# Performance work log

Hardware: AMD Instinct MI355X
Metric: run time of the kernel (lower is better)

The kernel has to match this reference:

```python
import jax, jax.numpy as jnp
import numpy as np

B, C_IMG, H, W = 16, 512, 32, 32
C_AUD, K_LEN, N_HEADS = 512, 256, 8
HEAD_DIM = C_AUD // N_HEADS
EPS = 1e-5


def setup_inputs() -> dict:
    key = jax.random.key(0)
    ks = jax.random.split(key, 12)
    s_img = 1.0 / np.sqrt(C_IMG)
    s_aud = 1.0 / np.sqrt(C_AUD)
    return {
        "img_feat": jax.random.normal(ks[0], (B, C_IMG, H, W), jnp.float32),
        "audio_feat": jax.random.normal(ks[1], (B, K_LEN, C_AUD), jnp.float32),
        "Wq": jax.random.uniform(ks[2], (C_IMG, C_AUD), jnp.float32, -s_img, s_img),
        "bq": jnp.zeros((C_AUD,), jnp.float32),
        "Wk": jax.random.uniform(ks[3], (C_AUD, C_AUD), jnp.float32, -s_aud, s_aud),
        "bk": jnp.zeros((C_AUD,), jnp.float32),
        "Wv": jax.random.uniform(ks[4], (C_AUD, C_AUD), jnp.float32, -s_aud, s_aud),
        "bv": jnp.zeros((C_AUD,), jnp.float32),
        "Wo": jax.random.uniform(ks[5], (C_AUD, C_IMG), jnp.float32, -s_aud, s_aud),
        "bo": jnp.zeros((C_IMG,), jnp.float32),
        "gamma": jnp.ones((C_IMG,), jnp.float32),
        "beta": jnp.zeros((C_IMG,), jnp.float32),
    }


def reference(img_feat, audio_feat, Wq, bq, Wk, bk, Wv, bv, Wo, bo, gamma, beta):
    b, c, h, w = img_feat.shape
    # b c h w -> b (h w) c
    img_seq = img_feat.reshape(b, c, h * w).transpose(0, 2, 1)
    q = img_seq @ Wq + bq                      # [b, q, C_AUD]
    k = audio_feat @ Wk + bk                   # [b, k, C_AUD]
    v = audio_feat @ Wv + bv
    # split heads: b s (h d) -> b h s d
    def split(x):
        bs, s, _ = x.shape
        return x.reshape(bs, s, N_HEADS, HEAD_DIM).transpose(0, 2, 1, 3)
    qh, kh, vh = split(q), split(k), split(v)
    scale = HEAD_DIM ** -0.5
    scores = jnp.einsum('bhqd,bhkd->bhqk', qh, kh) * scale
    weights = jax.nn.softmax(scores, axis=-1)
    attn = jnp.einsum('bhqk,bhkd->bhqd', weights, vh)
    attn = attn.transpose(0, 2, 1, 3).reshape(b, h * w, C_AUD)
    proj = attn @ Wo + bo                      # [b, q, C_IMG]
    y = img_seq + proj
    mu = jnp.mean(y, axis=-1, keepdims=True)
    var = jnp.mean((y - mu) ** 2, axis=-1, keepdims=True)
    y = (y - mu) * jax.lax.rsqrt(var + EPS) * gamma + beta
    # b (h w) c -> b c h w
    return y.transpose(0, 2, 1).reshape(b, c, h, w)
```

## Files before the change

kernel.cpp:

```cpp
#include <hip/hip_runtime.h>
#include <cstddef>

#define B_SZ 16
#define HW 1024
#define CCH 512
#define K_LEN 256
#define N_HEADS 8
#define EPS 1e-5f

typedef __bf16 bf16;
typedef bf16 bf16x8 __attribute__((ext_vector_type(8)));
typedef bf16 bf16x4 __attribute__((ext_vector_type(4)));
typedef float f32x4 __attribute__((ext_vector_type(4)));

__device__ __forceinline__ void gl_lds16(const bf16* g, bf16* l) {
    __builtin_amdgcn_global_load_lds(
        (const __attribute__((address_space(1))) void*)g,
        (__attribute__((address_space(3))) void*)l, 16, 0, 0);
}

__global__ __launch_bounds__(256) void transpose_cast_img(
    const float* __restrict__ src, bf16* __restrict__ dst)
{
    const int b  = blockIdx.z;
    const int s0 = blockIdx.x * 64;
    const int c0 = blockIdx.y * 64;
    __shared__ bf16 T[64][72];
    const int tid = threadIdx.x;
    {
        const int r = tid >> 2, cs = (tid & 3) << 4;
        const float* sp = src + ((size_t)b * CCH + c0 + r) * HW + s0 + cs;
        #pragma unroll
        for (int i = 0; i < 4; ++i) {
            float4 f = *(const float4*)(sp + i * 4);
            T[r][cs + i*4 + 0] = (bf16)f.x;
            T[r][cs + i*4 + 1] = (bf16)f.y;
            T[r][cs + i*4 + 2] = (bf16)f.z;
            T[r][cs + i*4 + 3] = (bf16)f.w;
        }
    }
    __syncthreads();
    {
        const int ss = tid >> 2, ks = (tid & 3) << 4;
        bf16x8 a, b8;
        #pragma unroll
        for (int j = 0; j < 8; ++j) { a[j] = T[ks + j][ss]; b8[j] = T[ks + 8 + j][ss]; }
        bf16* dp = dst + ((size_t)b * HW + s0 + ss) * CCH + c0 + ks;
        *(bf16x8*)dp = a;
        *(bf16x8*)(dp + 8) = b8;
    }
}

__global__ __launch_bounds__(256) void transpose_cast_w(
    const float* __restrict__ Wq, const float* __restrict__ Wk,
    const float* __restrict__ Wv, const float* __restrict__ Wo,
    bf16* __restrict__ dst)
{
    const int w = blockIdx.z;
    const float* src = (w == 0) ? Wq : (w == 1) ? Wk : (w == 2) ? Wv : Wo;
    const int n0 = blockIdx.x * 64;
    const int k0 = blockIdx.y * 64;
    __shared__ bf16 T[64][72];
    const int tid = threadIdx.x;
    {
        const int r = tid >> 2, cs = (tid & 3) << 4;
        const float* sp = src + (size_t)(k0 + r) * CCH + n0 + cs;
        #pragma unroll
        for (int i = 0; i < 4; ++i) {
            float4 f = *(const float4*)(sp + i * 4);
            T[r][cs + i*4 + 0] = (bf16)f.x;
            T[r][cs + i*4 + 1] = (bf16)f.y;
            T[r][cs + i*4 + 2] = (bf16)f.z;
            T[r][cs + i*4 + 3] = (bf16)f.w;
        }
    }
    __syncthreads();
    {
        const int nn = tid >> 2, ks = (tid & 3) << 4;
        bf16x8 a, b8;
        #pragma unroll
        for (int j = 0; j < 8; ++j) { a[j] = T[ks + j][nn]; b8[j] = T[ks + 8 + j][nn]; }
        bf16* dp = dst + (size_t)w * CCH * CCH + (size_t)(n0 + nn) * CCH + k0 + ks;
        *(bf16x8*)dp = a;
        *(bf16x8*)(dp + 8) = b8;
    }
}

__global__ __launch_bounds__(256) void gemm_bf16_mfma(
    const bf16* __restrict__ A, const bf16* __restrict__ Bt,
    const float* __restrict__ bias, bf16* __restrict__ out)
{
    const int tid  = threadIdx.x;
    const int wave = tid >> 6, lane = tid & 63;
    const int m0 = blockIdx.x * 128;
    const int n0 = blockIdx.y * 128;
    const int l15 = lane & 15, quad = lane >> 4;
    const int wm = (wave >> 1) * 64, wn = (wave & 1) * 64;

    __shared__ bf16 As[128 * 32];
    __shared__ bf16 Bs[128 * 32];

    const int r16 = lane >> 2;
    const int ks  = (lane & 3) * 8;

    f32x4 acc[4][4];
    #pragma unroll
    for (int i = 0; i < 4; ++i)
        #pragma unroll
        for (int j = 0; j < 4; ++j)
            acc[i][j] = (f32x4){0.f, 0.f, 0.f, 0.f};

    for (int k0 = 0; k0 < 512; k0 += 32) {
        #pragma unroll
        for (int i = 0; i < 2; ++i) {
            const int c = wave * 2 + i;
            gl_lds16(A  + (size_t)(m0 + c * 16 + r16) * 512 + k0 + ks, &As[c * 512]);
            gl_lds16(Bt + (size_t)(n0 + c * 16 + r16) * 512 + k0 + ks, &Bs[c * 512]);
        }
        __syncthreads();
        bf16x8 af[4], bfr[4];
        #pragma unroll
        for (int i = 0; i < 4; ++i)
            af[i] = *(const bf16x8*)&As[(wm + i * 16 + l15) * 32 + quad * 8];
        #pragma unroll
        for (int j = 0; j < 4; ++j)
            bfr[j] = *(const bf16x8*)&Bs[(wn + j * 16 + l15) * 32 + quad * 8];
        #pragma unroll
        for (int i = 0; i < 4; ++i)
            #pragma unroll
            for (int j = 0; j < 4; ++j)
                acc[i][j] = __builtin_amdgcn_mfma_f32_16x16x32_bf16(bfr[j], af[i], acc[i][j], 0, 0, 0);
        __syncthreads();
    }

    #pragma unroll
    for (int j = 0; j < 4; ++j) {
        const int gn = n0 + wn + j * 16 + quad * 4;
        const f32x4 bv4 = *(const f32x4*)(bias + gn);
        #pragma unroll
        for (int i = 0; i < 4; ++i) {
            const int gm = m0 + wm + i * 16 + l15;
            bf16x4 ov;
            #pragma unroll
            for (int r = 0; r < 4; ++r) ov[r] = (bf16)(acc[i][j][r] + bv4[r]);
            *(bf16x4*)(out + (size_t)gm * 512 + gn) = ov;
        }
    }
}

__global__ __launch_bounds__(256) void gemm_kv_mfma(
    const float* __restrict__ audio,
    const bf16* __restrict__ Bt,
    const float* __restrict__ bk, const float* __restrict__ bv,
    bf16* __restrict__ khout, bf16* __restrict__ vtout)
{
    const int tid  = threadIdx.x;
    const int wave = tid >> 6, lane = tid & 63;
    const int m0 = blockIdx.x * 128;
    const int n0 = blockIdx.y * 128;
    const int l15 = lane & 15, quad = lane >> 4;
    const int wm = (wave >> 1) * 64, wn = (wave & 1) * 64;

    __shared__ bf16 As[128 * 32];
    __shared__ bf16 Bs[128 * 32];

    const int r16 = lane >> 2;
    const int ks  = (lane & 3) * 8;

    f32x4 acc[4][4];
    #pragma unroll
    for (int i = 0; i < 4; ++i)
        #pragma unroll
        for (int j = 0; j < 4; ++j)
            acc[i][j] = (f32x4){0.f, 0.f, 0.f, 0.f};

    for (int k0 = 0; k0 < 512; k0 += 32) {
        #pragma unroll
        for (int i = 0; i < 2; ++i) {
            const int c = wave * 2 + i;
            gl_lds16(Bt + (size_t)(n0 + c * 16 + r16) * 512 + k0 + ks, &Bs[c * 512]);
        }
        #pragma unroll
        for (int i = 0; i < 2; ++i) {
            const int u = tid + (i << 8);
            const int r = u >> 2, seg = (u & 3) << 3;
            const float* ap = audio + (size_t)(m0 + r) * 512 + k0 + seg;
            f32x4 a0 = *(const f32x4*)ap;
            f32x4 a1 = *(const f32x4*)(ap + 4);
            bf16x8 o;
            #pragma unroll
            for (int q = 0; q < 4; ++q) { o[q] = (bf16)a0[q]; o[q + 4] = (bf16)a1[q]; }
            *(bf16x8*)&As[r * 32 + seg] = o;
        }
        __syncthreads();
        bf16x8 af[4], bfr[4];
        #pragma unroll
        for (int i = 0; i < 4; ++i)
            af[i] = *(const bf16x8*)&As[(wm + i * 16 + l15) * 32 + quad * 8];
        #pragma unroll
        for (int j = 0; j < 4; ++j)
            bfr[j] = *(const bf16x8*)&Bs[(wn + j * 16 + l15) * 32 + quad * 8];
        #pragma unroll
        for (int i = 0; i < 4; ++i)
            #pragma unroll
            for (int j = 0; j < 4; ++j)
                acc[i][j] = __builtin_amdgcn_mfma_f32_16x16x32_bf16(af[i], bfr[j], acc[i][j], 0, 0, 0);
        __syncthreads();
    }

    #pragma unroll
    for (int j = 0; j < 4; ++j) {
        const int gn = n0 + wn + j * 16 + l15;
        if (gn < 512) {
            const int h = gn >> 6, d = gn & 63;
            const float bias = bk[gn];
            #pragma unroll
            for (int i = 0; i < 4; ++i) {
                const int gm = m0 + wm + i * 16 + quad * 4;
                const int b = gm >> 8, key = gm & 255;
                bf16* base = khout + ((((size_t)b * N_HEADS + h) * K_LEN) + key) * 64 + d;
                #pragma unroll
                for (int r = 0; r < 4; ++r)
                    base[(size_t)r * 64] = (bf16)(acc[i][j][r] + bias);
            }
        } else {
            const int ch = gn - 512;
            const int h = ch >> 6, d = ch & 63;
            const float bias = bv[ch];
            #pragma unroll
            for (int i = 0; i < 4; ++i) {
                const int gm = m0 + wm + i * 16 + quad * 4;
                const int b = gm >> 8, key = gm & 255;
                bf16x4 pk;
                #pragma unroll
                for (int r = 0; r < 4; ++r) pk[r] = (bf16)(acc[i][j][r] + bias);
                *(bf16x4*)(vtout + (((size_t)b * N_HEADS + h) * 64 + d) * K_LEN + key) = pk;
            }
        }
    }
}

__global__ __launch_bounds__(256) void attn_mfma(
    const bf16* __restrict__ q,
    const bf16* __restrict__ kh,
    const bf16* __restrict__ vt,
    bf16* __restrict__ o)
{
    const int bh = blockIdx.x;
    const int s0 = blockIdx.y * 64;
    const int tid = threadIdx.x;
    const int wave = tid >> 6, lane = tid & 63;
    const int l15 = lane & 15, quad = lane >> 4;
    const int b = bh >> 3, h = bh & 7;

    __shared__ bf16 KsPt[18432];
    __shared__ bf16 Vs[16896];

    const bf16* khb = kh + (size_t)bh * K_LEN * 64;
    const bf16* vtb = vt + (size_t)bh * 64 * K_LEN;

    #pragma unroll
    for (int i = 0; i < 8; ++i) {
        const int chunk = tid + (i << 8);
        const int key = chunk >> 3, dseg = (chunk & 7) << 3;
        *(bf16x8*)&KsPt[key * 72 + dseg] = *(const bf16x8*)(khb + key * 64 + dseg);
        const int d = chunk >> 5, kseg = (chunk & 31) << 3;
        *(bf16x8*)&Vs[d * 264 + kseg] = *(const bf16x8*)(vtb + d * 256 + kseg);
    }
    __syncthreads();

    const int qrow = s0 + wave * 16 + l15;
    const bf16* qp = q + ((size_t)(b * HW + qrow)) * 512 + h * 64 + quad * 8;
    const bf16x8 qf0 = *(const bf16x8*)qp;
    const bf16x8 qf1 = *(const bf16x8*)(qp + 32);

    f32x4 acc[16];
    #pragma unroll
    for (int m = 0; m < 16; ++m) acc[m] = (f32x4){0.f, 0.f, 0.f, 0.f};
    #pragma unroll
    for (int m = 0; m < 16; ++m) {
        const bf16x8 a0 = *(const bf16x8*)&KsPt[(m * 16 + l15) * 72 + quad * 8];
        const bf16x8 a1 = *(const bf16x8*)&KsPt[(m * 16 + l15) * 72 + 32 + quad * 8];
        acc[m] = __builtin_amdgcn_mfma_f32_16x16x32_bf16(a0, qf0, acc[m], 0, 0, 0);
        acc[m] = __builtin_amdgcn_mfma_f32_16x16x32_bf16(a1, qf1, acc[m], 0, 0, 0);
    }

    float mx = -1e30f;
    #pragma unroll
    for (int m = 0; m < 16; ++m)
        mx = fmaxf(mx, fmaxf(fmaxf(acc[m][0], acc[m][1]), fmaxf(acc[m][2], acc[m][3])));
    mx = fmaxf(mx, __shfl_xor(mx, 16, 64));
    mx = fmaxf(mx, __shfl_xor(mx, 32, 64));

    __syncthreads();

    bf16* PtW = &KsPt[wave * 4224];
    float l_sum = 0.f;
    #pragma unroll
    for (int m = 0; m < 16; ++m) {
        bf16x4 pk;
        #pragma unroll
        for (int r = 0; r < 4; ++r) {
            const float p = __expf((acc[m][r] - mx) * 0.125f);
            l_sum += p;
            pk[r] = (bf16)p;
        }
        *(bf16x4*)&PtW[l15 * 264 + m * 16 + quad * 4] = pk;
    }
    l_sum += __shfl_xor(l_sum, 16, 64);
    l_sum += __shfl_xor(l_sum, 32, 64);
    __syncthreads();

    f32x4 oacc[4];
    #pragma unroll
    for (int m = 0; m < 4; ++m) oacc[m] = (f32x4){0.f, 0.f, 0.f, 0.f};
    #pragma unroll
    for (int s = 0; s < 8; ++s) {
        const bf16x8 pb = *(const bf16x8*)&PtW[l15 * 264 + s * 32 + quad * 8];
        #pragma unroll
        for (int m = 0; m < 4; ++m) {
            const bf16x8 va = *(const bf16x8*)&Vs[(m * 16 + l15) * 264 + s * 32 + quad * 8];
            oacc[m] = __builtin_amdgcn_mfma_f32_16x16x32_bf16(va, pb, oacc[m], 0, 0, 0);
        }
    }

    const float inv = 1.0f / l_sum;
    bf16* op = o + ((size_t)(b * HW + qrow)) * 512 + h * 64 + quad * 4;
    #pragma unroll
    for (int m = 0; m < 4; ++m) {
        bf16x4 ov;
        #pragma unroll
        for (int r = 0; r < 4; ++r) ov[r] = (bf16)(oacc[m][r] * inv);
        *(bf16x4*)&op[m * 16] = ov;
    }
}

__global__ __launch_bounds__(256) void gemm_oln(
    const bf16* __restrict__ A,
    const bf16* __restrict__ Wt,
    const float* __restrict__ bo,
    const float* __restrict__ img,
    const float* __restrict__ gamma, const float* __restrict__ beta,
    float* __restrict__ out)
{
    const int tid  = threadIdx.x;
    const int wave = tid >> 6, lane = tid & 63;
    const int l15 = lane & 15, quad = lane >> 4;
    const int m0 = blockIdx.x * 32;
    const int b  = m0 >> 10, s0 = m0 & 1023;
    const int wn = wave * 128;

    __shared__ bf16 As[32 * 32];
    __shared__ bf16 Bs[512 * 32];
    __shared__ float redS[2][32][4];

    const int r16 = lane >> 2;
    const int ks  = (lane & 3) * 8;

    f32x4 acc[2][8];
    #pragma unroll
    for (int i = 0; i < 2; ++i)
        #pragma unroll
        for (int j = 0; j < 8; ++j)
            acc[i][j] = (f32x4){0.f, 0.f, 0.f, 0.f};

    for (int k0 = 0; k0 < 512; k0 += 32) {
        #pragma unroll
        for (int t = 0; t < 8; ++t) {
            const int cb = wave * 8 + t;
            gl_lds16(Wt + (size_t)(cb * 16 + r16) * 512 + k0 + ks, &Bs[cb * 512]);
        }
        if (wave < 2)
            gl_lds16(A + (size_t)(m0 + wave * 16 + r16) * 512 + k0 + ks, &As[wave * 512]);
        __syncthreads();
        bf16x8 af[2], bfr[8];
        #pragma unroll
        for (int i = 0; i < 2; ++i)
            af[i] = *(const bf16x8*)&As[(i * 16 + l15) * 32 + quad * 8];
        #pragma unroll
        for (int j = 0; j < 8; ++j)
            bfr[j] = *(const bf16x8*)&Bs[(wn + j * 16 + l15) * 32 + quad * 8];
        #pragma unroll
        for (int i = 0; i < 2; ++i)
            #pragma unroll
            for (int j = 0; j < 8; ++j)
                acc[i][j] = __builtin_amdgcn_mfma_f32_16x16x32_bf16(af[i], bfr[j], acc[i][j], 0, 0, 0);
        __syncthreads();
    }

    float rs_[2][4] = {}, rq_[2][4] = {};
    #pragma unroll
    for (int j = 0; j < 8; ++j) {
        const int c = wn + j * 16 + l15;
        const float bo_c = bo[c];
        #pragma unroll
        for (int i = 0; i < 2; ++i) {
            const int sb = s0 + i * 16 + quad * 4;
            const f32x4 res = *(const f32x4*)(img + ((size_t)b * CCH + c) * HW + sb);
            #pragma unroll
            for (int r = 0; r < 4; ++r) {
                const float y = acc[i][j][r] + bo_c + res[r];
                acc[i][j][r] = y;
                rs_[i][r] += y;
                rq_[i][r] += y * y;
            }
        }
    }
    #pragma unroll
    for (int i = 0; i < 2; ++i)
        #pragma unroll
        for (int r = 0; r < 4; ++r) {
            #pragma unroll
            for (int m = 1; m < 16; m <<= 1) {
                rs_[i][r] += __shfl_xor(rs_[i][r], m, 64);
                rq_[i][r] += __shfl_xor(rq_[i][r], m, 64);
            }
        }
    if (l15 == 0) {
        #pragma unroll
        for (int i = 0; i < 2; ++i)
            #pragma unroll
            for (int r = 0; r < 4; ++r) {
                redS[0][i * 16 + quad * 4 + r][wave] = rs_[i][r];
                redS[1][i * 16 + quad * 4 + r][wave] = rq_[i][r];
            }
    }
    __syncthreads();

    float mu[2][4], rstd[2][4];
    #pragma unroll
    for (int i = 0; i < 2; ++i)
        #pragma unroll
        for (int r = 0; r < 4; ++r) {
            const int s = i * 16 + quad * 4 + r;
            const float sm = redS[0][s][0] + redS[0][s][1] + redS[0][s][2] + redS[0][s][3];
            const float sq = redS[1][s][0] + redS[1][s][1] + redS[1][s][2] + redS[1][s][3];
            const float m_ = sm * (1.f / 512.f);
            mu[i][r] = m_;
            rstd[i][r] = rsqrtf(sq * (1.f / 512.f) - m_ * m_ + EPS);
        }

    #pragma unroll
    for (int j = 0; j < 8; ++j) {
        const int c = wn + j * 16 + l15;
        const float g_c = gamma[c];
        const float be_c = beta[c];
        #pragma unroll
        for (int i = 0; i < 2; ++i) {
            const int sb = s0 + i * 16 + quad * 4;
            f32x4 z;
            #pragma unroll
            for (int r = 0; r < 4; ++r)
                z[r] = (acc[i][j][r] - mu[i][r]) * rstd[i][r] * g_c + be_c;
            *(f32x4*)(out + ((size_t)b * CCH + c) * HW + sb) = z;
        }
    }
}

extern "C" void kernel_launch(void* const* d_in, const int* in_sizes, int n_in,
                              void* d_out, int out_size, void* d_ws, size_t ws_size,
                              hipStream_t stream) {
    const float* img   = (const float*)d_in[0];
    const float* audio = (const float*)d_in[1];
    const float* Wq    = (const float*)d_in[2];
    const float* bq    = (const float*)d_in[3];
    const float* Wk    = (const float*)d_in[4];
    const float* bk    = (const float*)d_in[5];
    const float* Wv    = (const float*)d_in[6];
    const float* bv    = (const float*)d_in[7];
    const float* Wo    = (const float*)d_in[8];
    const float* bo    = (const float*)d_in[9];
    const float* gamma = (const float*)d_in[10];
    const float* beta  = (const float*)d_in[11];

    bf16* wsb    = (bf16*)d_ws;
    bf16* img_bf = wsb;
    bf16* wT     = img_bf + 8388608;
    bf16* q_bf   = wT + 1048576;
    bf16* kh_bf  = q_bf + 8388608;
    bf16* vt_bf  = kh_bf + 2097152;
    bf16* a_bf   = vt_bf + 2097152;

    transpose_cast_img<<<dim3(16, 8, 16), 256, 0, stream>>>(img, img_bf);
    transpose_cast_w<<<dim3(8, 8, 4), 256, 0, stream>>>(Wq, Wk, Wv, Wo, wT);

    gemm_bf16_mfma<<<dim3(128, 4), 256, 0, stream>>>(img_bf, wT, bq, q_bf);
    gemm_kv_mfma<<<dim3(32, 8), 256, 0, stream>>>(audio, wT + 262144, bk, bv, kh_bf, vt_bf);
    attn_mfma<<<dim3(B_SZ * N_HEADS, HW / 64), 256, 0, stream>>>(q_bf, kh_bf, vt_bf, a_bf);
    gemm_oln<<<dim3(512), 256, 0, stream>>>(a_bf, wT + 3 * 262144, bo, img, gamma, beta, (float*)d_out);
}
```

Before: 204.2 us.

## Merge transpose and QKV launches, keep K in registers, read bf16 residual

Merges the two transpose-cast kernels into one launch and the Q and KV projection GEMMs into one launch, cutting the launch count from six to four. The attention kernel now holds K fragments in registers, stages P in shared memory per wave and loops over several query tiles per block, so each block loads K and V once for more queries. The output/LayerNorm kernel reads the residual from the bf16 transposed image instead of fp32 and uses a transposed MFMA layout, giving vector bias/gamma loads but scalar strided output stores. The bf16 residual reduces precision of the skip path.

```diff
diff --git a/kernel.cpp b/kernel.cpp
--- a/kernel.cpp
+++ b/kernel.cpp
@@ -19,90 +19,87 @@
         (__attribute__((address_space(3))) void*)l, 16, 0, 0);
 }
 
-__global__ __launch_bounds__(256) void transpose_cast_img(
-    const float* __restrict__ src, bf16* __restrict__ dst)
+__global__ __launch_bounds__(256) void tc_all(
+    const float* __restrict__ img,
+    const float* __restrict__ Wq, const float* __restrict__ Wk,
+    const float* __restrict__ Wv, const float* __restrict__ Wo,
+    bf16* __restrict__ img_bf, bf16* __restrict__ wT)
 {
-    const int b  = blockIdx.z;
-    const int s0 = blockIdx.x * 64;
-    const int c0 = blockIdx.y * 64;
     __shared__ bf16 T[64][72];
     const int tid = threadIdx.x;
-    {
-        const int r = tid >> 2, cs = (tid & 3) << 4;
-        const float* sp = src + ((size_t)b * CCH + c0 + r) * HW + s0 + cs;
-        #pragma unroll
-        for (int i = 0; i < 4; ++i) {
-            float4 f = *(const float4*)(sp + i * 4);
-            T[r][cs + i*4 + 0] = (bf16)f.x;
-            T[r][cs + i*4 + 1] = (bf16)f.y;
-            T[r][cs + i*4 + 2] = (bf16)f.z;
-            T[r][cs + i*4 + 3] = (bf16)f.w;
-        }
-    }
-    __syncthreads();
-    {
-        const int ss = tid >> 2, ks = (tid & 3) << 4;
-        bf16x8 a, b8;
-        #pragma unroll
-        for (int j = 0; j < 8; ++j) { a[j] = T[ks + j][ss]; b8[j] = T[ks + 8 + j][ss]; }
-        bf16* dp = dst + ((size_t)b * HW + s0 + ss) * CCH + c0 + ks;
-        *(bf16x8*)dp = a;
-        *(bf16x8*)(dp + 8) = b8;
-    }
-}
-
-__global__ __launch_bounds__(256) void transpose_cast_w(
-    const float* __restrict__ Wq, const float* __restrict__ Wk,
-    const float* __restrict__ Wv, const float* __restrict__ Wo,
-    bf16* __restrict__ dst)
+    const int z = blockIdx.z;
+    if (z < 16) {
+        const int b = z, s0 = blockIdx.x * 64, c0 = blockIdx.y * 64;
+        {
+            const int r = tid >> 2, cs = (tid & 3) << 4;
+            const float* sp = img + ((size_t)b * CCH + c0 + r) * HW + s0 + cs;
+            #pragma unroll
+            for (int i = 0; i < 4; ++i) {
+                float4 f = *(const float4*)(sp + i * 4);
+                T[r][cs + i*4 + 0] = (bf16)f.x;
+                T[r][cs + i*4 + 1] = (bf16)f.y;
+                T[r][cs + i*4 + 2] = (bf16)f.z;
+                T[r][cs + i*4 + 3] = (bf16)f.w;
+            }
+        }
+        __syncthreads();
+        {
+            const int ss = tid >> 2, ks = (tid & 3) << 4;
+            bf16x8 a, b8;
+            #pragma unroll
+            for (int j = 0; j < 8; ++j) { a[j] = T[ks + j][ss]; b8[j] = T[ks + 8 + j][ss]; }
+            bf16* dp = img_bf + ((size_t)b * HW + s0 + ss) * CCH + c0 + ks;
+            *(bf16x8*)dp = a;
+            *(bf16x8*)(dp + 8) = b8;
+        }
+    } else {
+        if (blockIdx.x >= 8) return;
+        const int w = z - 16;
+        const float* src = (w == 0) ? Wq : (w == 1) ? Wk : (w == 2) ? Wv : Wo;
+        const int n0 = blockIdx.x * 64, k0 = blockIdx.y * 64;
+        {
+            const int r = tid >> 2, cs = (tid & 3) << 4;
+            const float* sp = src + (size_t)(k0 + r) * CCH + n0 + cs;
+            #pragma unroll
+            for (int i = 0; i < 4; ++i) {
+                float4 f = *(const float4*)(sp + i * 4);
+                T[r][cs + i*4 + 0] = (bf16)f.x;
+                T[r][cs + i*4 + 1] = (bf16)f.y;
+                T[r][cs + i*4 + 2] = (bf16)f.z;
+                T[r][cs + i*4 + 3] = (bf16)f.w;
+            }
+        }
+        __syncthreads();
+        {
+            const int nn = tid >> 2, ks = (tid & 3) << 4;
+            bf16x8 a, b8;
+            #pragma unroll
+            for (int j = 0; j < 8; ++j) { a[j] = T[ks + j][nn]; b8[j] = T[ks + 8 + j][nn]; }
+            bf16* dp = wT + (size_t)w * CCH * CCH + (size_t)(n0 + nn) * CCH + k0 + ks;
+            *(bf16x8*)dp = a;
+            *(bf16x8*)(dp + 8) = b8;
+        }
+    }
+}
+
+__global__ __launch_bounds__(256) void gemm_qkv(
+    const bf16* __restrict__ img_bf, const float* __restrict__ audio,
+    const bf16* __restrict__ wT,
+    const float* __restrict__ bq, const float* __restrict__ bk,
+    const float* __restrict__ bv,
+    bf16* __restrict__ q_bf, bf16* __restrict__ khout, bf16* __restrict__ vtout)
 {
-    const int w = blockIdx.z;
-    const float* src = (w == 0) ? Wq : (w == 1) ? Wk : (w == 2) ? Wv : Wo;
-    const int n0 = blockIdx.x * 64;
-    const int k0 = blockIdx.y * 64;
-    __shared__ bf16 T[64][72];
+    const int bid = blockIdx.x;
     const int tid = threadIdx.x;
-    {
-        const int r = tid >> 2, cs = (tid & 3) << 4;
-        const float* sp = src + (size_t)(k0 + r) * CCH + n0 + cs;
-        #pragma unroll
-        for (int i = 0; i < 4; ++i) {
-            float4 f = *(const float4*)(sp + i * 4);
-            T[r][cs + i*4 + 0] = (bf16)f.x;
-            T[r][cs + i*4 + 1] = (bf16)f.y;
-            T[r][cs + i*4 + 2] = (bf16)f.z;
-            T[r][cs + i*4 + 3] = (bf16)f.w;
-        }
-    }
-    __syncthreads();
-    {
-        const int nn = tid >> 2, ks = (tid & 3) << 4;
-        bf16x8 a, b8;
-        #pragma unroll
-        for (int j = 0; j < 8; ++j) { a[j] = T[ks + j][nn]; b8[j] = T[ks + 8 + j][nn]; }
-        bf16* dp = dst + (size_t)w * CCH * CCH + (size_t)(n0 + nn) * CCH + k0 + ks;
-        *(bf16x8*)dp = a;
-        *(bf16x8*)(dp + 8) = b8;
-    }
-}
-
-__global__ __launch_bounds__(256) void gemm_bf16_mfma(
-    const bf16* __restrict__ A, const bf16* __restrict__ Bt,
-    const float* __restrict__ bias, bf16* __restrict__ out)
-{
-    const int tid  = threadIdx.x;
     const int wave = tid >> 6, lane = tid & 63;
-    const int m0 = blockIdx.x * 128;
-    const int n0 = blockIdx.y * 128;
     const int l15 = lane & 15, quad = lane >> 4;
     const int wm = (wave >> 1) * 64, wn = (wave & 1) * 64;
+    const int r16 = lane >> 2;
+    const int ks  = (lane & 3) * 8;
 
     __shared__ bf16 As[128 * 32];
     __shared__ bf16 Bs[128 * 32];
 
-    const int r16 = lane >> 2;
-    const int ks  = (lane & 3) * 8;
-
     f32x4 acc[4][4];
     #pragma unroll
     for (int i = 0; i < 4; ++i)
@@ -110,151 +107,128 @@
         for (int j = 0; j < 4; ++j)
             acc[i][j] = (f32x4){0.f, 0.f, 0.f, 0.f};
 
-    for (int k0 = 0; k0 < 512; k0 += 32) {
-        #pragma unroll
-        for (int i = 0; i < 2; ++i) {
-            const int c = wave * 2 + i;
-            gl_lds16(A  + (size_t)(m0 + c * 16 + r16) * 512 + k0 + ks, &As[c * 512]);
-            gl_lds16(Bt + (size_t)(n0 + c * 16 + r16) * 512 + k0 + ks, &Bs[c * 512]);
-        }
-        __syncthreads();
-        bf16x8 af[4], bfr[4];
-        #pragma unroll
-        for (int i = 0; i < 4; ++i)
-            af[i] = *(const bf16x8*)&As[(wm + i * 16 + l15) * 32 + quad * 8];
-        #pragma unroll
-        for (int j = 0; j < 4; ++j)
-            bfr[j] = *(const bf16x8*)&Bs[(wn + j * 16 + l15) * 32 + quad * 8];
-        #pragma unroll
-        for (int i = 0; i < 4; ++i)
+    if (bid < 512) {
+        const int m0 = (bid >> 2) * 128, n0 = (bid & 3) * 128;
+        for (int k0 = 0; k0 < 512; k0 += 32) {
+            #pragma unroll
+            for (int i = 0; i < 2; ++i) {
+                const int c = wave * 2 + i;
+                gl_lds16(img_bf + (size_t)(m0 + c * 16 + r16) * 512 + k0 + ks, &As[c * 512]);
+                gl_lds16(wT     + (size_t)(n0 + c * 16 + r16) * 512 + k0 + ks, &Bs[c * 512]);
+            }
+            __syncthreads();
+            bf16x8 af[4], bfr[4];
+            #pragma unroll
+            for (int i = 0; i < 4; ++i)
+                af[i] = *(const bf16x8*)&As[(wm + i * 16 + l15) * 32 + quad * 8];
             #pragma unroll
             for (int j = 0; j < 4; ++j)
-                acc[i][j] = __builtin_amdgcn_mfma_f32_16x16x32_bf16(bfr[j], af[i], acc[i][j], 0, 0, 0);
-        __syncthreads();
-    }
-
-    #pragma unroll
-    for (int j = 0; j < 4; ++j) {
-        const int gn = n0 + wn + j * 16 + quad * 4;
-        const f32x4 bv4 = *(const f32x4*)(bias + gn);
-        #pragma unroll
-        for (int i = 0; i < 4; ++i) {
-            const int gm = m0 + wm + i * 16 + l15;
-            bf16x4 ov;
-            #pragma unroll
-            for (int r = 0; r < 4; ++r) ov[r] = (bf16)(acc[i][j][r] + bv4[r]);
-            *(bf16x4*)(out + (size_t)gm * 512 + gn) = ov;
-        }
-    }
-}
-
-__global__ __launch_bounds__(256) void gemm_kv_mfma(
-    const float* __restrict__ audio,
-    const bf16* __restrict__ Bt,
-    const float* __restrict__ bk, const float* __restrict__ bv,
-    bf16* __restrict__ khout, bf16* __restrict__ vtout)
-{
-    const int tid  = threadIdx.x;
-    const int wave = tid >> 6, lane = tid & 63;
-    const int m0 = blockIdx.x * 128;
-    const int n0 = blockIdx.y * 128;
-    const int l15 = lane & 15, quad = lane >> 4;
-    const int wm = (wave >> 1) * 64, wn = (wave & 1) * 64;
-
-    __shared__ bf16 As[128 * 32];
-    __shared__ bf16 Bs[128 * 32];
-
-    const int r16 = lane >> 2;
-    const int ks  = (lane & 3) * 8;
-
-    f32x4 acc[4][4];
-    #pragma unroll
-    for (int i = 0; i < 4; ++i)
-        #pragma unroll
-        for (int j = 0; j < 4; ++j)
-            acc[i][j] = (f32x4){0.f, 0.f, 0.f, 0.f};
-
-    for (int k0 = 0; k0 < 512; k0 += 32) {
-        #pragma unroll
-        for (int i = 0; i < 2; ++i) {
-            const int c = wave * 2 + i;
-            gl_lds16(Bt + (size_t)(n0 + c * 16 + r16) * 512 + k0 + ks, &Bs[c * 512]);
-        }
-        #pragma unroll
-        for (int i = 0; i < 2; ++i) {
-            const int u = tid + (i << 8);
-            const int r = u >> 2, seg = (u & 3) << 3;
-            const float* ap = audio + (size_t)(m0 + r) * 512 + k0 + seg;
-            f32x4 a0 = *(const f32x4*)ap;
-            f32x4 a1 = *(const f32x4*)(ap + 4);
-            bf16x8 o;
-            #pragma unroll
-            for (int q = 0; q < 4; ++q) { o[q] = (bf16)a0[q]; o[q + 4] = (bf16)a1[q]; }
-            *(bf16x8*)&As[r * 32 + seg] = o;
-        }
-        __syncthreads();
-        bf16x8 af[4], bfr[4];
-        #pragma unroll
-        for (int i = 0; i < 4; ++i)
-            af[i] = *(const bf16x8*)&As[(wm + i * 16 + l15) * 32 + quad * 8];
-        #pragma unroll
-        for (int j = 0; j < 4; ++j)
-            bfr[j] = *(const bf16x8*)&Bs[(wn + j * 16 + l15) * 32 + quad * 8];
-        #pragma unroll
-        for (int i = 0; i < 4; ++i)
+                bfr[j] = *(const bf16x8*)&Bs[(wn + j * 16 + l15) * 32 + quad * 8];
+            #pragma unroll
+            for (int i = 0; i < 4; ++i)
+                #pragma unroll
+                for (int j = 0; j < 4; ++j)
+                    acc[i][j] = __builtin_amdgcn_mfma_f32_16x16x32_bf16(bfr[j], af[i], acc[i][j], 0, 0, 0);
+            __syncthreads();
+        }
+        #pragma unroll
+        for (int j = 0; j < 4; ++j) {
+            const int gn = n0 + wn + j * 16 + quad * 4;
+            const f32x4 bv4 = *(const f32x4*)(bq + gn);
+            #pragma unroll
+            for (int i = 0; i < 4; ++i) {
+                const int gm = m0 + wm + i * 16 + l15;
+                bf16x4 ov;
+                #pragma unroll
+                for (int r = 0; r < 4; ++r) ov[r] = (bf16)(acc[i][j][r] + bv4[r]);
+                *(bf16x4*)(q_bf + (size_t)gm * 512 + gn) = ov;
+            }
+        }
+    } else {
+        const int t = bid - 512;
+        const int m0 = (t >> 3) * 128, n0 = (t & 7) * 128;
+        const bf16* Bt = wT + 262144;
+        for (int k0 = 0; k0 < 512; k0 += 32) {
+            #pragma unroll
+            for (int i = 0; i < 2; ++i) {
+                const int c = wave * 2 + i;
+                gl_lds16(Bt + (size_t)(n0 + c * 16 + r16) * 512 + k0 + ks, &Bs[c * 512]);
+            }
+            #pragma unroll
+            for (int i = 0; i < 2; ++i) {
+                const int u = tid + (i << 8);
+                const int r = u >> 2, seg = (u & 3) << 3;
+                const float* ap = audio + (size_t)(m0 + r) * 512 + k0 + seg;
+                f32x4 a0 = *(const f32x4*)ap;
+                f32x4 a1 = *(const f32x4*)(ap + 4);
+                bf16x8 o;
+                #pragma unroll
+                for (int qq = 0; qq < 4; ++qq) { o[qq] = (bf16)a0[qq]; o[qq + 4] = (bf16)a1[qq]; }
+                *(bf16x8*)&As[r * 32 + seg] = o;
+            }
+            __syncthreads();
+            bf16x8 af[4], bfr[4];
+            #pragma unroll
+            for (int i = 0; i < 4; ++i)
+                af[i] = *(const bf16x8*)&As[(wm + i * 16 + l15) * 32 + quad * 8];
             #pragma unroll
             for (int j = 0; j < 4; ++j)
-                acc[i][j] = __builtin_amdgcn_mfma_f32_16x16x32_bf16(af[i], bfr[j], acc[i][j], 0, 0, 0);
-        __syncthreads();
-    }
-
-    #pragma unroll
-    for (int j = 0; j < 4; ++j) {
-        const int gn = n0 + wn + j * 16 + l15;
-        if (gn < 512) {
-            const int h = gn >> 6, d = gn & 63;
-            const float bias = bk[gn];
-            #pragma unroll
-            for (int i = 0; i < 4; ++i) {
-                const int gm = m0 + wm + i * 16 + quad * 4;
-                const int b = gm >> 8, key = gm & 255;
-                bf16* base = khout + ((((size_t)b * N_HEADS + h) * K_LEN) + key) * 64 + d;
-                #pragma unroll
-                for (int r = 0; r < 4; ++r)
-                    base[(size_t)r * 64] = (bf16)(acc[i][j][r] + bias);
-            }
-        } else {
-            const int ch = gn - 512;
-            const int h = ch >> 6, d = ch & 63;
-            const float bias = bv[ch];
-            #pragma unroll
-            for (int i = 0; i < 4; ++i) {
-                const int gm = m0 + wm + i * 16 + quad * 4;
-                const int b = gm >> 8, key = gm & 255;
-                bf16x4 pk;
-                #pragma unroll
-                for (int r = 0; r < 4; ++r) pk[r] = (bf16)(acc[i][j][r] + bias);
-                *(bf16x4*)(vtout + (((size_t)b * N_HEADS + h) * 64 + d) * K_LEN + key) = pk;
-            }
-        }
-    }
-}
-
-__global__ __launch_bounds__(256) void attn_mfma(
+                bfr[j] = *(const bf16x8*)&Bs[(wn + j * 16 + l15) * 32 + quad * 8];
+            #pragma unroll
+            for (int i = 0; i < 4; ++i)
+                #pragma unroll
+                for (int j = 0; j < 4; ++j)
+                    acc[i][j] = __builtin_amdgcn_mfma_f32_16x16x32_bf16(af[i], bfr[j], acc[i][j], 0, 0, 0);
+            __syncthreads();
+        }
+        #pragma unroll
+        for (int j = 0; j < 4; ++j) {
+            const int gn = n0 + wn + j * 16 + l15;
+            if (gn < 512) {
+                const int h = gn >> 6, d = gn & 63;
+                const float bias = bk[gn];
+                #pragma unroll
+                for (int i = 0; i < 4; ++i) {
+                    const int gm = m0 + wm + i * 16 + quad * 4;
+                    const int b = gm >> 8, key = gm & 255;
+                    bf16* base = khout + ((((size_t)b * N_HEADS + h) * K_LEN) + key) * 64 + d;
+                    #pragma unroll
+                    for (int r = 0; r < 4; ++r)
+                        base[(size_t)r * 64] = (bf16)(acc[i][j][r] + bias);
+                }
+            } else {
+                const int ch = gn - 512;
+                const int h = ch >> 6, d = ch & 63;
+                const float bias = bv[ch];
+                #pragma unroll
+                for (int i = 0; i < 4; ++i) {
+                    const int gm = m0 + wm + i * 16 + quad * 4;
+                    const int b = gm >> 8, key = gm & 255;
+                    bf16x4 pk;
+                    #pragma unroll
+                    for (int r = 0; r < 4; ++r) pk[r] = (bf16)(acc[i][j][r] + bias);
+                    *(bf16x4*)(vtout + (((size_t)b * N_HEADS + h) * 64 + d) * K_LEN + key) = pk;
+                }
+            }
+        }
+    }
+}
+
+__global__ __launch_bounds__(256, 2) void attn_mfma(
     const bf16* __restrict__ q,
     const bf16* __restrict__ kh,
     const bf16* __restrict__ vt,
     bf16* __restrict__ o)
 {
     const int bh = blockIdx.x;
-    const int s0 = blockIdx.y * 64;
+    const int sg = blockIdx.y;
     const int tid = threadIdx.x;
     const int wave = tid >> 6, lane = tid & 63;
     const int l15 = lane & 15, quad = lane >> 4;
     const int b = bh >> 3, h = bh & 7;
 
-    __shared__ bf16 KsPt[18432];
-    __shared__ bf16 Vs[16896];
+    __shared__ bf16 Vs[64 * 264];
+    __shared__ bf16 Pt[4 * 16 * 264];
 
     const bf16* khb = kh + (size_t)bh * K_LEN * 64;
     const bf16* vtb = vt + (size_t)bh * 64 * K_LEN;
@@ -262,76 +236,79 @@
     #pragma unroll
     for (int i = 0; i < 8; ++i) {
         const int chunk = tid + (i << 8);
-        const int key = chunk >> 3, dseg = (chunk & 7) << 3;
-        *(bf16x8*)&KsPt[key * 72 + dseg] = *(const bf16x8*)(khb + key * 64 + dseg);
         const int d = chunk >> 5, kseg = (chunk & 31) << 3;
         *(bf16x8*)&Vs[d * 264 + kseg] = *(const bf16x8*)(vtb + d * 256 + kseg);
     }
+    bf16x8 kf0[16], kf1[16];
+    #pragma unroll
+    for (int m = 0; m < 16; ++m) {
+        const bf16* kp = khb + (size_t)(m * 16 + l15) * 64 + quad * 8;
+        kf0[m] = *(const bf16x8*)kp;
+        kf1[m] = *(const bf16x8*)(kp + 32);
+    }
     __syncthreads();
 
-    const int qrow = s0 + wave * 16 + l15;
-    const bf16* qp = q + ((size_t)(b * HW + qrow)) * 512 + h * 64 + quad * 8;
-    const bf16x8 qf0 = *(const bf16x8*)qp;
-    const bf16x8 qf1 = *(const bf16x8*)(qp + 32);
-
-    f32x4 acc[16];
-    #pragma unroll
-    for (int m = 0; m < 16; ++m) acc[m] = (f32x4){0.f, 0.f, 0.f, 0.f};
-    #pragma unroll
-    for (int m = 0; m < 16; ++m) {
-        const bf16x8 a0 = *(const bf16x8*)&KsPt[(m * 16 + l15) * 72 + quad * 8];
-        const bf16x8 a1 = *(const bf16x8*)&KsPt[(m * 16 + l15) * 72 + 32 + quad * 8];
-        acc[m] = __builtin_amdgcn_mfma_f32_16x16x32_bf16(a0, qf0, acc[m], 0, 0, 0);
-        acc[m] = __builtin_amdgcn_mfma_f32_16x16x32_bf16(a1, qf1, acc[m], 0, 0, 0);
-    }
-
-    float mx = -1e30f;
-    #pragma unroll
-    for (int m = 0; m < 16; ++m)
-        mx = fmaxf(mx, fmaxf(fmaxf(acc[m][0], acc[m][1]), fmaxf(acc[m][2], acc[m][3])));
-    mx = fmaxf(mx, __shfl_xor(mx, 16, 64));
-    mx = fmaxf(mx, __shfl_xor(mx, 32, 64));
-
-    __syncthreads();
-
-    bf16* PtW = &KsPt[wave * 4224];
-    float l_sum = 0.f;
-    #pragma unroll
-    for (int m = 0; m < 16; ++m) {
-        bf16x4 pk;
-        #pragma unroll
-        for (int r = 0; r < 4; ++r) {
-            const float p = __expf((acc[m][r] - mx) * 0.125f);
-            l_sum += p;
-            pk[r] = (bf16)p;
-        }
-        *(bf16x4*)&PtW[l15 * 264 + m * 16 + quad * 4] = pk;
-    }
-    l_sum += __shfl_xor(l_sum, 16, 64);
-    l_sum += __shfl_xor(l_sum, 32, 64);
-    __syncthreads();
-
-    f32x4 oacc[4];
-    #pragma unroll
-    for (int m = 0; m < 4; ++m) oacc[m] = (f32x4){0.f, 0.f, 0.f, 0.f};
-    #pragma unroll
-    for (int s = 0; s < 8; ++s) {
-        const bf16x8 pb = *(const bf16x8*)&PtW[l15 * 264 + s * 32 + quad * 8];
+    bf16* PtW = &Pt[wave * 4224];
+
+    for (int it = 0; it < 4; ++it) {
+        const int qrow = sg * 256 + it * 64 + wave * 16 + l15;
+        const bf16* qp = q + ((size_t)(b * HW + qrow)) * 512 + h * 64 + quad * 8;
+        const bf16x8 qf0 = *(const bf16x8*)qp;
+        const bf16x8 qf1 = *(const bf16x8*)(qp + 32);
+
+        f32x4 acc[16];
+        #pragma unroll
+        for (int m = 0; m < 16; ++m) acc[m] = (f32x4){0.f, 0.f, 0.f, 0.f};
+        #pragma unroll
+        for (int m = 0; m < 16; ++m) {
+            acc[m] = __builtin_amdgcn_mfma_f32_16x16x32_bf16(kf0[m], qf0, acc[m], 0, 0, 0);
+            acc[m] = __builtin_amdgcn_mfma_f32_16x16x32_bf16(kf1[m], qf1, acc[m], 0, 0, 0);
+        }
+
+        float mx = -1e30f;
+        #pragma unroll
+        for (int m = 0; m < 16; ++m)
+            mx = fmaxf(mx, fmaxf(fmaxf(acc[m][0], acc[m][1]), fmaxf(acc[m][2], acc[m][3])));
+        mx = fmaxf(mx, __shfl_xor(mx, 16, 64));
+        mx = fmaxf(mx, __shfl_xor(mx, 32, 64));
+
+        float l_sum = 0.f;
+        #pragma unroll
+        for (int m = 0; m < 16; ++m) {
+            bf16x4 pk;
+            #pragma unroll
+            for (int r = 0; r < 4; ++r) {
+                const float p = __expf((acc[m][r] - mx) * 0.125f);
+                l_sum += p;
+                pk[r] = (bf16)p;
+            }
+            *(bf16x4*)&PtW[l15 * 264 + m * 16 + quad * 4] = pk;
+        }
+        l_sum += __shfl_xor(l_sum, 16, 64);
+        l_sum += __shfl_xor(l_sum, 32, 64);
+
+        f32x4 oacc[4];
+        #pragma unroll
+        for (int m = 0; m < 4; ++m) oacc[m] = (f32x4){0.f, 0.f, 0.f, 0.f};
+        #pragma unroll
+        for (int s = 0; s < 8; ++s) {
+            const bf16x8 pb = *(const bf16x8*)&PtW[l15 * 264 + s * 32 + quad * 8];
+            #pragma unroll
+            for (int m = 0; m < 4; ++m) {
+                const bf16x8 va = *(const bf16x8*)&Vs[(m * 16 + l15) * 264 + s * 32 + quad * 8];
+                oacc[m] = __builtin_amdgcn_mfma_f32_16x16x32_bf16(va, pb, oacc[m], 0, 0, 0);
+            }
+        }
+
+        const float inv = 1.0f / l_sum;
+        bf16* op = o + ((size_t)(b * HW + qrow)) * 512 + h * 64 + quad * 4;
         #pragma unroll
         for (int m = 0; m < 4; ++m) {
-            const bf16x8 va = *(const bf16x8*)&Vs[(m * 16 + l15) * 264 + s * 32 + quad * 8];
-            oacc[m] = __builtin_amdgcn_mfma_f32_16x16x32_bf16(va, pb, oacc[m], 0, 0, 0);
-        }
-    }
-
-    const float inv = 1.0f / l_sum;
-    bf16* op = o + ((size_t)(b * HW + qrow)) * 512 + h * 64 + quad * 4;
-    #pragma unroll
-    for (int m = 0; m < 4; ++m) {
-        bf16x4 ov;
-        #pragma unroll
-        for (int r = 0; r < 4; ++r) ov[r] = (bf16)(oacc[m][r] * inv);
-        *(bf16x4*)&op[m * 16] = ov;
+            bf16x4 ov;
+            #pragma unroll
+            for (int r = 0; r < 4; ++r) ov[r] = (bf16)(oacc[m][r] * inv);
+            *(bf16x4*)&op[m * 16] = ov;
+        }
     }
 }
 
@@ -339,7 +316,7 @@
     const bf16* __restrict__ A,
     const bf16* __restrict__ Wt,
     const float* __restrict__ bo,
-    const float* __restrict__ img,
+    const bf16* __restrict__ imgb,
     const float* __restrict__ gamma, const float* __restrict__ beta,
     float* __restrict__ out)
 {
@@ -384,75 +361,65 @@
         for (int i = 0; i < 2; ++i)
             #pragma unroll
             for (int j = 0; j < 8; ++j)
-                acc[i][j] = __builtin_amdgcn_mfma_f32_16x16x32_bf16(af[i], bfr[j], acc[i][j], 0, 0, 0);
+                acc[i][j] = __builtin_amdgcn_mfma_f32_16x16x32_bf16(bfr[j], af[i], acc[i][j], 0, 0, 0);
         __syncthreads();
     }
 
-    float rs_[2][4] = {}, rq_[2][4] = {};
+    float rs_[2] = {0.f, 0.f}, rq_[2] = {0.f, 0.f};
     #pragma unroll
     for (int j = 0; j < 8; ++j) {
-        const int c = wn + j * 16 + l15;
-        const float bo_c = bo[c];
+        const int c4 = wn + j * 16 + quad * 4;
+        const f32x4 bo4 = *(const f32x4*)(bo + c4);
         #pragma unroll
         for (int i = 0; i < 2; ++i) {
-            const int sb = s0 + i * 16 + quad * 4;
-            const f32x4 res = *(const f32x4*)(img + ((size_t)b * CCH + c) * HW + sb);
+            const bf16x4 res = *(const bf16x4*)(imgb + (size_t)(m0 + i * 16 + l15) * 512 + c4);
             #pragma unroll
             for (int r = 0; r < 4; ++r) {
-                const float y = acc[i][j][r] + bo_c + res[r];
+                const float y = acc[i][j][r] + bo4[r] + (float)res[r];
                 acc[i][j][r] = y;
-                rs_[i][r] += y;
-                rq_[i][r] += y * y;
-            }
-        }
-    }
-    #pragma unroll
-    for (int i = 0; i < 2; ++i)
-        #pragma unroll
-        for (int r = 0; r < 4; ++r) {
-            #pragma unroll
-            for (int m = 1; m < 16; m <<= 1) {
-                rs_[i][r] += __shfl_xor(rs_[i][r], m, 64);
-                rq_[i][r] += __shfl_xor(rq_[i][r], m, 64);
-            }
-        }
-    if (l15 == 0) {
-        #pragma unroll
-        for (int i = 0; i < 2; ++i)
+                rs_[i] += y;
+                rq_[i] += y * y;
+            }
+        }
+    }
+    #pragma unroll
+    for (int i = 0; i < 2; ++i) {
+        rs_[i] += __shfl_xor(rs_[i], 16, 64);
+        rs_[i] += __shfl_xor(rs_[i], 32, 64);
+        rq_[i] += __shfl_xor(rq_[i], 16, 64);
+        rq_[i] += __shfl_xor(rq_[i], 32, 64);
+    }
+    if (quad == 0) {
+        #pragma unroll
+        for (int i = 0; i < 2; ++i) {
+            redS[0][i * 16 + l15][wave] = rs_[i];
+            redS[1][i * 16 + l15][wave] = rq_[i];
+        }
+    }
+    __syncthreads();
+
+    float mu[2], rstd[2];
+    #pragma unroll
+    for (int i = 0; i < 2; ++i) {
+        const int s = i * 16 + l15;
+        const float sm = redS[0][s][0] + redS[0][s][1] + redS[0][s][2] + redS[0][s][3];
+        const float sq = redS[1][s][0] + redS[1][s][1] + redS[1][s][2] + redS[1][s][3];
+        mu[i] = sm * (1.f / 512.f);
+        rstd[i] = rsqrtf(sq * (1.f / 512.f) - mu[i] * mu[i] + EPS);
+    }
+
+    #pragma unroll
+    for (int j = 0; j < 8; ++j) {
+        const int c4 = wn + j * 16 + quad * 4;
+        const f32x4 g4 = *(const f32x4*)(gamma + c4);
+        const f32x4 b4 = *(const f32x4*)(beta + c4);
+        #pragma unroll
+        for (int i = 0; i < 2; ++i) {
             #pragma unroll
             for (int r = 0; r < 4; ++r) {
-                redS[0][i * 16 + quad * 4 + r][wave] = rs_[i][r];
-                redS[1][i * 16 + quad * 4 + r][wave] = rq_[i][r];
-            }
-    }
-    __syncthreads();
-
-    float mu[2][4], rstd[2][4];
-    #pragma unroll
-    for (int i = 0; i < 2; ++i)
-        #pragma unroll
-        for (int r = 0; r < 4; ++r) {
-            const int s = i * 16 + quad * 4 + r;
-            const float sm = redS[0][s][0] + redS[0][s][1] + redS[0][s][2] + redS[0][s][3];
-            const float sq = redS[1][s][0] + redS[1][s][1] + redS[1][s][2] + redS[1][s][3];
-            const float m_ = sm * (1.f / 512.f);
-            mu[i][r] = m_;
-            rstd[i][r] = rsqrtf(sq * (1.f / 512.f) - m_ * m_ + EPS);
-        }
-
-    #pragma unroll
-    for (int j = 0; j < 8; ++j) {
-        const int c = wn + j * 16 + l15;
-        const float g_c = gamma[c];
-        const float be_c = beta[c];
-        #pragma unroll
-        for (int i = 0; i < 2; ++i) {
-            const int sb = s0 + i * 16 + quad * 4;
-            f32x4 z;
-            #pragma unroll
-            for (int r = 0; r < 4; ++r)
-                z[r] = (acc[i][j][r] - mu[i][r]) * rstd[i][r] * g_c + be_c;
-            *(f32x4*)(out + ((size_t)b * CCH + c) * HW + sb) = z;
+                const float z = (acc[i][j][r] - mu[i]) * rstd[i] * g4[r] + b4[r];
+                out[((size_t)b * CCH + c4 + r) * HW + s0 + i * 16 + l15] = z;
+            }
         }
     }
 }
@@ -481,11 +448,10 @@
     bf16* vt_bf  = kh_bf + 2097152;
     bf16* a_bf   = vt_bf + 2097152;
 
-    transpose_cast_img<<<dim3(16, 8, 16), 256, 0, stream>>>(img, img_bf);
-    transpose_cast_w<<<dim3(8, 8, 4), 256, 0, stream>>>(Wq, Wk, Wv, Wo, wT);
-
-    gemm_bf16_mfma<<<dim3(128, 4), 256, 0, stream>>>(img_bf, wT, bq, q_bf);
-    gemm_kv_mfma<<<dim3(32, 8), 256, 0, stream>>>(audio, wT + 262144, bk, bv, kh_bf, vt_bf);
-    attn_mfma<<<dim3(B_SZ * N_HEADS, HW / 64), 256, 0, stream>>>(q_bf, kh_bf, vt_bf, a_bf);
-    gemm_oln<<<dim3(512), 256, 0, stream>>>(a_bf, wT + 3 * 262144, bo, img, gamma, beta, (float*)d_out);
-}
+    tc_all<<<dim3(16, 8, 20), 256, 0, stream>>>(img, Wq, Wk, Wv, Wo, img_bf, wT);
+    gemm_qkv<<<dim3(768), 256, 0, stream>>>(img_bf, audio, wT, bq, bk, bv,
+                                            q_bf, kh_bf, vt_bf);
+    attn_mfma<<<dim3(B_SZ * N_HEADS, 4), 256, 0, stream>>>(q_bf, kh_bf, vt_bf, a_bf);
+    gemm_oln<<<dim3(512), 256, 0, stream>>>(a_bf, wT + 3 * 262144, bo, img_bf,
+                                            gamma, beta, (float*)d_out);
+}
```

Result: slower. 224.0 us (+9.7%).
